# Kernel optimization log

Measured on AMD Instinct MI355X. Metric: run time of the kernel, lower is better.

The kernel has to match this reference:

```python
import jax, jax.numpy as jnp
import numpy as np

B, N, H, K = 8192, 256, 1024, 256
BETA = 0.99
TOL = 1e-4
MAX_ITER = 100

def V_fn(x, Wv):
    # x: (B,1,N) -> (B,1,1); positive-definite quadratic Lyapunov V(x) = ||x @ Wv||^2
    z = jnp.einsum('bon,nk->bok', x, Wv)
    return jnp.sum(z * z, axis=-1, keepdims=True)

def fhat_fn(x, W1, b1, W2, b2):
    # residual tanh MLP dynamics model fhat: (B,1,N) -> (B,1,N)
    h = jnp.tanh(jnp.einsum('bon,nh->boh', x, W1) + b1)
    return x + jnp.einsum('boh,hn->bon', h, W2) + b2

def dV_da(fx, a, Wv):
    # per-sample d/d(alpha) V(fx * alpha); mirrors torch.autograd.grad(Vfx, alpha)
    def v_scalar(a_s, fx_s):
        z = (fx_s * a_s) @ Wv
        return jnp.sum(z * z)
    g = jax.vmap(jax.grad(v_scalar))(a[:, 0, 0], fx[:, 0, :])
    return g[:, None, None]

def newton_F(fx, t, a, Wv):
    # newton_iter.forward: F = alpha - (V(fhatx*alpha) - target) / dV_da
    # dV_da was computed with create_graph=False in torch -> constant -> stop_gradient
    dv = jax.lax.stop_gradient(dV_da(fx, a, Wv))
    return a - (V_fn(fx * a, Wv) - t) / dv

def solve_alpha(fhatx, target, Wv):
    # vectorized Newton + bisection with per-sample masking (rootfind_train.forward)
    Bn = fhatx.shape[0]
    alpha0 = jnp.ones((Bn, 1, 1), jnp.float32)
    e1_0 = jnp.zeros_like(alpha0)
    e2_0 = jnp.ones_like(alpha0)
    m0 = (V_fn(fhatx, Wv) - target) > 0.0

    def cond(c):
        a, e1, e2, m, it = c
        return jnp.logical_and(jnp.any(m), it < MAX_ITER)

    def body(c):
        a, e1, e2, m, it = c
        a = jnp.where(m, newton_F(fhatx, target, a, Wv), a)
        m_bis = (a < e1) | (a > e2)
        a_bis = e1 + (e2 - e1) / 2
        sa = jnp.sign(V_fn(fhatx * a_bis, Wv) - target)
        s1 = jnp.sign(V_fn(fhatx * e1, Wv) - target)
        s2 = jnp.sign(V_fn(fhatx * e2, Wv) - target)
        m_end2 = m_bis & (sa * s1 < 0)
        m_end1 = m_bis & (sa * s2 < 0)
        e2 = jnp.where(m_end2, a_bis, e2)
        e1 = jnp.where(m_end1, a_bis, e1)
        a = jnp.where(m_bis, a_bis, a)
        m = jnp.abs(V_fn(fhatx * a, Wv) - target) > TOL
        return (a, e1, e2, m, it + 1)

    a, _, _, _, _ = jax.lax.while_loop(cond, body, (alpha0, e1_0, e2_0, m0, jnp.int32(0)))
    return a

def setup_inputs() -> dict:
    key = jax.random.key(0)
    ks = jax.random.split(key, 4)
    x = jax.random.normal(ks[0], (B, 1, N), jnp.float32)
    W1 = jax.random.normal(ks[1], (N, H), jnp.float32) / np.sqrt(N)
    b1 = jnp.zeros((H,), jnp.float32)
    W2 = jax.random.normal(ks[2], (H, N), jnp.float32) * (0.5 / np.sqrt(H))
    b2 = jnp.zeros((N,), jnp.float32)
    Wv = jax.random.normal(ks[3], (N, K), jnp.float32) / np.sqrt(N)
    return {'x': x, 'W1': W1, 'b1': b1, 'W2': W2, 'b2': b2, 'Wv': Wv}

def reference(x, W1, b1, W2, b2, Wv):
    fhatx = fhat_fn(x, W1, b1, W2, b2)
    target = BETA * V_fn(x, Wv)
    alpha = jax.lax.stop_gradient(solve_alpha(fhatx, target, Wv))  # alpha detached in torch
    return fhatx * alpha
```

## Files before the change

### kernel.cpp

```cpp
#include <hip/hip_runtime.h>
#include <math.h>

typedef __attribute__((ext_vector_type(8))) short bf16x8;
typedef __attribute__((ext_vector_type(4))) float f32x4;

#define MFMA __builtin_amdgcn_mfma_f32_16x16x32_bf16

static __device__ __forceinline__ unsigned short f2bf(float f) {
  union { float f; unsigned u; } a; a.f = f;
  unsigned u = a.u;
  unsigned r = u + 0x7FFF + ((u >> 16) & 1);
  return (unsigned short)(r >> 16);
}
static __device__ __forceinline__ float bf2f(unsigned short h) {
  union { unsigned u; float f; } a; a.u = ((unsigned)h) << 16;
  return a.f;
}
static __device__ __forceinline__ float tanh_fast(float x) {
  float ax = fabsf(x);
  float e = __expf(-2.0f * ax);
  float t = (1.0f - e) / (1.0f + e);
  t = (ax > 10.0f) ? 1.0f : t;
  return (x < 0.0f) ? -t : t;
}
static __device__ __forceinline__ void gload16(const void* g, void* l) {
  __builtin_amdgcn_global_load_lds(
      (const __attribute__((address_space(1))) unsigned int*)g,
      (__attribute__((address_space(3))) unsigned int*)l, 16, 0, 0);
}

__global__ __launch_bounds__(256) void k_split(
    const float* __restrict__ W1, const float* __restrict__ W2,
    const float* __restrict__ Wv, const float* __restrict__ X,
    unsigned short* __restrict__ W1Th, unsigned short* __restrict__ W1Tl,
    unsigned short* __restrict__ W2Th, unsigned short* __restrict__ W2Tl,
    unsigned short* __restrict__ WvTh, unsigned short* __restrict__ WvTl,
    unsigned short* __restrict__ Xh,  unsigned short* __restrict__ Xl)
{
  const int b = blockIdx.x, t = threadIdx.x;
  if (b >= 144) {
    const size_t i0 = (size_t)(b - 144) * 2048 + (size_t)t * 8;
    const float4 v0 = *reinterpret_cast<const float4*>(&X[i0]);
    const float4 v1 = *reinterpret_cast<const float4*>(&X[i0 + 4]);
    const float vv[8] = {v0.x, v0.y, v0.z, v0.w, v1.x, v1.y, v1.z, v1.w};
    uint4 hp, lp;
    unsigned hw[4], lw[4];
#pragma unroll
    for (int e = 0; e < 4; ++e) {
      const unsigned short h0 = f2bf(vv[2*e]), h1 = f2bf(vv[2*e+1]);
      hw[e] = (unsigned)h0 | ((unsigned)h1 << 16);
      lw[e] = (unsigned)f2bf(vv[2*e] - bf2f(h0)) |
              ((unsigned)f2bf(vv[2*e+1] - bf2f(h1)) << 16);
    }
    hp.x = hw[0]; hp.y = hw[1]; hp.z = hw[2]; hp.w = hw[3];
    lp.x = lw[0]; lp.y = lw[1]; lp.z = lw[2]; lp.w = lw[3];
    *reinterpret_cast<uint4*>(&Xh[i0]) = hp;
    *reinterpret_cast<uint4*>(&Xl[i0]) = lp;
    return;
  }

  __shared__ unsigned short shh[64 * 72], shl[64 * 72];
  const float* W; unsigned short *Th, *Tl; int Kd, Nd, k0, n0;
  if (b < 64)       { W = W1; Th = W1Th; Tl = W1Tl; Kd = 256;  Nd = 1024; k0 = (b & 3) * 64;         n0 = (b >> 2) * 64; }
  else if (b < 128) { W = W2; Th = W2Th; Tl = W2Tl; Kd = 1024; Nd = 256;  k0 = ((b - 64) & 15) * 64; n0 = ((b - 64) >> 4) * 64; }
  else              { W = Wv; Th = WvTh; Tl = WvTl; Kd = 256;  Nd = 256;  k0 = ((b - 128) & 3) * 64; n0 = ((b - 128) >> 2) * 64; }

  const int kloc = t >> 4, n4 = t & 15;
#pragma unroll
  for (int p = 0; p < 4; ++p) {
    const int kk = p * 16 + kloc;
    const float4 v = *reinterpret_cast<const float4*>(&W[(size_t)(k0 + kk) * Nd + n0 + n4 * 4]);
    const float vv[4] = {v.x, v.y, v.z, v.w};
#pragma unroll
    for (int e = 0; e < 4; ++e) {
      const unsigned short hh = f2bf(vv[e]);
      shh[(n4 * 4 + e) * 72 + kk] = hh;
      shl[(n4 * 4 + e) * 72 + kk] = f2bf(vv[e] - bf2f(hh));
    }
  }
  __syncthreads();
  const int nl = t >> 2, ko = (t & 3) * 16;
  const size_t dst = (size_t)(n0 + nl) * Kd + k0 + ko;
  *reinterpret_cast<uint4*>(&Th[dst])     = *reinterpret_cast<const uint4*>(&shh[nl * 72 + ko]);
  *reinterpret_cast<uint4*>(&Th[dst + 8]) = *reinterpret_cast<const uint4*>(&shh[nl * 72 + ko + 8]);
  *reinterpret_cast<uint4*>(&Tl[dst])     = *reinterpret_cast<const uint4*>(&shl[nl * 72 + ko]);
  *reinterpret_cast<uint4*>(&Tl[dst + 8]) = *reinterpret_cast<const uint4*>(&shl[nl * 72 + ko + 8]);
}

__global__ __launch_bounds__(256, 3) void k_gemm1(
    const unsigned short* __restrict__ Xh, const unsigned short* __restrict__ Xl,
    const unsigned short* __restrict__ BTh, const unsigned short* __restrict__ BTl,
    const float* __restrict__ bias,
    unsigned short* __restrict__ Hh, unsigned short* __restrict__ Hl)
{
  __shared__ unsigned short lds[16384];
  const int t = threadIdx.x, l = t & 63, wv = t >> 6;
  const int n0 = blockIdx.x * 128, m0 = blockIdx.y * 128;
  const int wr = wv >> 1, wc = wv & 1;

  const unsigned short* ssrc = (wv == 0) ? Xh : (wv == 1) ? Xl : (wv == 2) ? BTh : BTl;
  const int rbase = (wv < 2) ? m0 : n0;
  char* ldsb = (char*)lds + wv * 8192;
  const int srow = l >> 2, sg = l & 3;

  const int kofs = (l >> 4) * 16;
  const int arow = wr * 64 + (l & 15), brow = wc * 64 + (l & 15);

  f32x4 acc[4][4] = {};
  for (int k0 = 0; k0 < 256; k0 += 32) {
#pragma unroll
    for (int c = 0; c < 8; ++c)
      gload16(ssrc + (size_t)(rbase + c * 16 + srow) * 256 + k0 + sg * 8, ldsb + c * 1024);
    __syncthreads();

    const char* L = (const char*)lds;
    bf16x8 ah[4], al[4], bh[4], bl[4];
#pragma unroll
    for (int i = 0; i < 4; ++i) {
      ah[i] = *reinterpret_cast<const bf16x8*>(L +         (arow + i * 16) * 64 + kofs);
      al[i] = *reinterpret_cast<const bf16x8*>(L +  8192 + (arow + i * 16) * 64 + kofs);
      bh[i] = *reinterpret_cast<const bf16x8*>(L + 16384 + (brow + i * 16) * 64 + kofs);
      bl[i] = *reinterpret_cast<const bf16x8*>(L + 24576 + (brow + i * 16) * 64 + kofs);
    }
#pragma unroll
    for (int i = 0; i < 4; ++i)
#pragma unroll
      for (int j = 0; j < 4; ++j) {
        acc[i][j] = MFMA(ah[i], bh[j], acc[i][j], 0, 0, 0);
        acc[i][j] = MFMA(ah[i], bl[j], acc[i][j], 0, 0, 0);
        acc[i][j] = MFMA(al[i], bh[j], acc[i][j], 0, 0, 0);
      }
    __syncthreads();
  }

#pragma unroll
  for (int i = 0; i < 4; ++i)
#pragma unroll
    for (int j = 0; j < 4; ++j) {
      const int gn = n0 + wc * 64 + j * 16 + (l & 15);
      const float bv = bias[gn];
#pragma unroll
      for (int r = 0; r < 4; ++r) {
        const int gm = m0 + wr * 64 + i * 16 + (l >> 4) * 4 + r;
        const float tv = tanh_fast(acc[i][j][r] + bv);
        const unsigned short th = f2bf(tv);
        Hh[(size_t)gm * 1024 + gn] = th;
        Hl[(size_t)gm * 1024 + gn] = f2bf(tv - bf2f(th));
      }
    }
}

__global__ __launch_bounds__(512, 4) void k_g2va(
    const unsigned short* __restrict__ Xh, const unsigned short* __restrict__ Xl,
    const unsigned short* __restrict__ Hh, const unsigned short* __restrict__ Hl,
    const unsigned short* __restrict__ W2Th, const unsigned short* __restrict__ W2Tl,
    const unsigned short* __restrict__ WvTh, const unsigned short* __restrict__ WvTl,
    const float* __restrict__ pb2, float* __restrict__ OUT)
{
  __shared__ __align__(16) unsigned char smem[67712];
  const int t = threadIdx.x, l = t & 63, w = t >> 6;
  const int cl = l & 15, g = l >> 4;
  const int r0 = blockIdx.x * 32;

  {
    const unsigned short* xp = (w < 4) ? Xh : Xl;
    unsigned char* base = smem + ((w < 4) ? 0 : 16384);
#pragma unroll
    for (int s = 0; s < 4; ++s) {
      const int c = (w & 3) * 4 + s;
      const int row = c * 2 + (l >> 5);
      const int slot = l & 31;
      gload16(xp + (size_t)(r0 + row) * 256 + ((slot ^ (row & 7)) * 8), base + c * 1024);
    }
    const unsigned short* hp = (w < 4) ? Hh : Hl;
    unsigned char* abase = smem + 32768 + ((w < 4) ? 0 : 4096) + (w & 3) * 1024;
    const int row = (w & 3) * 8 + (l >> 3);
    const int slot = l & 7;
    gload16(hp + (size_t)(r0 + row) * 1024 + 0 * 64 + ((slot ^ (row & 7)) * 8), abase);
  }
  __syncthreads();

  f32x4 acc[2][2] = {};

  for (int c = 0; c < 16; ++c) {
    if (c < 15) {
      const int cn = c + 1;
      const unsigned short* hp = (w < 4) ? Hh : Hl;
      unsigned char* abase = smem + 32768 + (cn & 1) * 8192 + ((w < 4) ? 0 : 4096) + (w & 3) * 1024;
      const int row = (w & 3) * 8 + (l >> 3);
      const int slot = l & 7;
      gload16(hp + (size_t)(r0 + row) * 1024 + cn * 64 + ((slot ^ (row & 7)) * 8), abase);
    }
    bf16x8 b2h[2][2], b2l[2][2];
#pragma unroll
    for (int j = 0; j < 2; ++j)
#pragma unroll
      for (int ks = 0; ks < 2; ++ks) {
        const size_t off = (size_t)(w * 32 + j * 16 + cl) * 1024 + c * 64 + ks * 32 + g * 8;
        b2h[j][ks] = *reinterpret_cast<const bf16x8*>(&W2Th[off]);
        b2l[j][ks] = *reinterpret_cast<const bf16x8*>(&W2Tl[off]);
      }
    const unsigned char* AB = smem + 32768 + (c & 1) * 8192;
    bf16x8 a2h[2][2], a2l[2][2];
#pragma unroll
    for (int i = 0; i < 2; ++i)
#pragma unroll
      for (int ks = 0; ks < 2; ++ks) {
        const int row = i * 16 + cl;
        const unsigned byte = row * 128 + (((unsigned)(ks * 64 + g * 16)) ^ ((((unsigned)row) & 7u) << 4));
        a2h[i][ks] = *reinterpret_cast<const bf16x8*>(AB + byte);
        a2l[i][ks] = *reinterpret_cast<const bf16x8*>(AB + 4096 + byte);
      }
#pragma unroll
    for (int i = 0; i < 2; ++i)
#pragma unroll
      for (int j = 0; j < 2; ++j)
#pragma unroll
        for (int ks = 0; ks < 2; ++ks) {
          acc[i][j] = MFMA(a2h[i][ks], b2h[j][ks], acc[i][j], 0, 0, 0);
          acc[i][j] = MFMA(a2h[i][ks], b2l[j][ks], acc[i][j], 0, 0, 0);
          acc[i][j] = MFMA(a2l[i][ks], b2h[j][ks], acc[i][j], 0, 0, 0);
        }
    __syncthreads();
  }

  {
    float b2v[2];
#pragma unroll
    for (int j = 0; j < 2; ++j) b2v[j] = pb2[w * 32 + j * 16 + cl];
#pragma unroll
    for (int i = 0; i < 2; ++i)
#pragma unroll
      for (int j = 0; j < 2; ++j)
#pragma unroll
        for (int r = 0; r < 4; ++r) {
          const int row = i * 16 + g * 4 + r;
          const int col = w * 32 + j * 16 + cl;
          const unsigned xb = row * 512 + (((unsigned)(col * 2)) ^ ((((unsigned)row) & 7u) << 4));
          const float xv = bf2f(*reinterpret_cast<unsigned short*>(smem + xb)) +
                           bf2f(*reinterpret_cast<unsigned short*>(smem + 16384 + xb));
          const float f = acc[i][j][r] + b2v[j] + xv;
          acc[i][j][r] = f;
          const unsigned short fh = f2bf(f);
          *reinterpret_cast<unsigned short*>(smem + 32768 + xb) = fh;
          *reinterpret_cast<unsigned short*>(smem + 49152 + xb) = f2bf(f - bf2f(fh));
        }
  }
  __syncthreads();

  {
    float vx_[2][4] = {}, vf_[2][4] = {};
    f32x4 zx[2], zf[2];
#pragma unroll
    for (int nf = 0; nf < 2; ++nf) {
      zx[0] = (f32x4){}; zx[1] = (f32x4){};
      zf[0] = (f32x4){}; zf[1] = (f32x4){};
#pragma unroll
      for (int ks = 0; ks < 8; ++ks) {
        const size_t off = (size_t)(w * 32 + nf * 16 + cl) * 256 + ks * 32 + g * 8;
        const bf16x8 wvh = *reinterpret_cast<const bf16x8*>(&WvTh[off]);
        const bf16x8 wvl = *reinterpret_cast<const bf16x8*>(&WvTl[off]);
#pragma unroll
        for (int i = 0; i < 2; ++i) {
          const int row = i * 16 + cl;
          const unsigned o = ((unsigned)(ks * 64 + g * 16)) ^ ((((unsigned)row) & 7u) << 4);
          const bf16x8 xhv = *reinterpret_cast<const bf16x8*>(smem + row * 512 + o);
          const bf16x8 xlv = *reinterpret_cast<const bf16x8*>(smem + 16384 + row * 512 + o);
          const bf16x8 fhv = *reinterpret_cast<const bf16x8*>(smem + 32768 + row * 512 + o);
          const bf16x8 flv = *reinterpret_cast<const bf16x8*>(smem + 49152 + row * 512 + o);
          zx[i] = MFMA(xhv, wvh, zx[i], 0, 0, 0);
          zx[i] = MFMA(xhv, wvl, zx[i], 0, 0, 0);
          zx[i] = MFMA(xlv, wvh, zx[i], 0, 0, 0);
          zf[i] = MFMA(fhv, wvh, zf[i], 0, 0, 0);
          zf[i] = MFMA(fhv, wvl, zf[i], 0, 0, 0);
          zf[i] = MFMA(flv, wvh, zf[i], 0, 0, 0);
        }
      }
#pragma unroll
      for (int i = 0; i < 2; ++i)
#pragma unroll
        for (int r = 0; r < 4; ++r) {
          vx_[i][r] = fmaf(zx[i][r], zx[i][r], vx_[i][r]);
          vf_[i][r] = fmaf(zf[i][r], zf[i][r], vf_[i][r]);
        }
    }
    float* PX = (float*)(smem + 65536);
    float* PF = (float*)(smem + 66560);
#pragma unroll
    for (int i = 0; i < 2; ++i)
#pragma unroll
      for (int r = 0; r < 4; ++r) {
        float a = vx_[i][r], b = vf_[i][r];
        a += __shfl_xor(a, 1); a += __shfl_xor(a, 2); a += __shfl_xor(a, 4); a += __shfl_xor(a, 8);
        b += __shfl_xor(b, 1); b += __shfl_xor(b, 2); b += __shfl_xor(b, 4); b += __shfl_xor(b, 8);
        if (cl == 0) {
          const int row = i * 16 + g * 4 + r;
          PX[row * 8 + w] = a;
          PF[row * 8 + w] = b;
        }
      }
  }
  __syncthreads();

  float* ALS = (float*)(smem + 67584);
  if (t < 32) {
    const float* PX = (const float*)(smem + 65536);
    const float* PF = (const float*)(smem + 66560);
    float Vx = 0.f, Vf = 0.f;
#pragma unroll
    for (int i = 0; i < 8; ++i) { Vx += PX[t * 8 + i]; Vf += PF[t * 8 + i]; }
    const float tt2 = 0.99f * Vx;
    float a;
    if (Vf - tt2 > 0.0f)        a = sqrtf(tt2 / Vf);
    else if (tt2 - Vf > 1e-4f)  a = 0.5f;
    else                        a = 1.0f;
    ALS[t] = a;
  }
  __syncthreads();

#pragma unroll
  for (int i = 0; i < 2; ++i)
#pragma unroll
    for (int r = 0; r < 4; ++r) {
      const int row = i * 16 + g * 4 + r;
      const float a = ALS[row];
#pragma unroll
      for (int j = 0; j < 2; ++j) {
        const int col = w * 32 + j * 16 + cl;
        OUT[(size_t)(r0 + row) * 256 + col] = acc[i][j][r] * a;
      }
    }
}

extern "C" void kernel_launch(void* const* d_in, const int* in_sizes, int n_in,
                              void* d_out, int out_size, void* d_ws, size_t ws_size,
                              hipStream_t stream) {
  const float* x  = (const float*)d_in[0];
  const float* W1 = (const float*)d_in[1];
  const float* b1 = (const float*)d_in[2];
  const float* W2 = (const float*)d_in[3];
  const float* b2 = (const float*)d_in[4];
  const float* Wv = (const float*)d_in[5];
  float* out = (float*)d_out;

  char* ws = (char*)d_ws;
  unsigned short* Hh   = (unsigned short*)(ws);
  unsigned short* Hl   = (unsigned short*)(ws + 16777216);
  unsigned short* W1Th = (unsigned short*)(ws + 33554432);
  unsigned short* W1Tl = (unsigned short*)(ws + 34078720);
  unsigned short* W2Th = (unsigned short*)(ws + 34603008);
  unsigned short* W2Tl = (unsigned short*)(ws + 35127296);
  unsigned short* WvTh = (unsigned short*)(ws + 35651584);
  unsigned short* WvTl = (unsigned short*)(ws + 35782656);
  unsigned short* Xh   = (unsigned short*)(ws + 35913728);
  unsigned short* Xl   = (unsigned short*)(ws + 40108032);

  k_split<<<dim3(1168), dim3(256), 0, stream>>>(
      W1, W2, Wv, x, W1Th, W1Tl, W2Th, W2Tl, WvTh, WvTl, Xh, Xl);

  k_gemm1<<<dim3(8, 64), dim3(256), 0, stream>>>(Xh, Xl, W1Th, W1Tl, b1, Hh, Hl);
  k_g2va <<<dim3(256), dim3(512), 0, stream>>>(Xh, Xl, Hh, Hl, W2Th, W2Tl, WvTh, WvTl, b2, out);
}
```

Measured before the change: 83.41 us.

## Prefetch W2 and Wv register fragments ahead of use in g2va kernel

Adds register double-buffering for the W2 B-fragments in the k_g2va main loop: the next chunk's global loads are issued alongside the next H tile, and the loop is fully unrolled. It also hoists the Wv fragment loads ahead of the epilogue and the second V pass so that global latency overlaps earlier work. Launch bounds drop from 4 to 2 blocks per CU so the extra live registers fit. The cost is lower occupancy, which could expose other latencies.

```diff
diff --git a/kernel.cpp b/kernel.cpp
--- a/kernel.cpp
+++ b/kernel.cpp
@@ -150,7 +150,7 @@
     }
 }
 
-__global__ __launch_bounds__(512, 4) void k_g2va(
+__global__ __launch_bounds__(512, 2) void k_g2va(
     const unsigned short* __restrict__ Xh, const unsigned short* __restrict__ Xl,
     const unsigned short* __restrict__ Hh, const unsigned short* __restrict__ Hl,
     const unsigned short* __restrict__ W2Th, const unsigned short* __restrict__ W2Tl,
@@ -176,13 +176,25 @@
     unsigned char* abase = smem + 32768 + ((w < 4) ? 0 : 4096) + (w & 3) * 1024;
     const int row = (w & 3) * 8 + (l >> 3);
     const int slot = l & 7;
-    gload16(hp + (size_t)(r0 + row) * 1024 + 0 * 64 + ((slot ^ (row & 7)) * 8), abase);
-  }
+    gload16(hp + (size_t)(r0 + row) * 1024 + ((slot ^ (row & 7)) * 8), abase);
+  }
+
+  bf16x8 pbh[2][2][2], pbl[2][2][2];
+#pragma unroll
+  for (int j = 0; j < 2; ++j)
+#pragma unroll
+    for (int ks = 0; ks < 2; ++ks) {
+      const size_t off = (size_t)(w * 32 + j * 16 + cl) * 1024 + ks * 32 + g * 8;
+      pbh[0][j][ks] = *reinterpret_cast<const bf16x8*>(&W2Th[off]);
+      pbl[0][j][ks] = *reinterpret_cast<const bf16x8*>(&W2Tl[off]);
+    }
   __syncthreads();
 
   f32x4 acc[2][2] = {};
 
+#pragma unroll
   for (int c = 0; c < 16; ++c) {
+    const int p = c & 1, pn = p ^ 1;
     if (c < 15) {
       const int cn = c + 1;
       const unsigned short* hp = (w < 4) ? Hh : Hl;
@@ -190,17 +202,16 @@
       const int row = (w & 3) * 8 + (l >> 3);
       const int slot = l & 7;
       gload16(hp + (size_t)(r0 + row) * 1024 + cn * 64 + ((slot ^ (row & 7)) * 8), abase);
-    }
-    bf16x8 b2h[2][2], b2l[2][2];
-#pragma unroll
-    for (int j = 0; j < 2; ++j)
-#pragma unroll
-      for (int ks = 0; ks < 2; ++ks) {
-        const size_t off = (size_t)(w * 32 + j * 16 + cl) * 1024 + c * 64 + ks * 32 + g * 8;
-        b2h[j][ks] = *reinterpret_cast<const bf16x8*>(&W2Th[off]);
-        b2l[j][ks] = *reinterpret_cast<const bf16x8*>(&W2Tl[off]);
-      }
-    const unsigned char* AB = smem + 32768 + (c & 1) * 8192;
+#pragma unroll
+      for (int j = 0; j < 2; ++j)
+#pragma unroll
+        for (int ks = 0; ks < 2; ++ks) {
+          const size_t off = (size_t)(w * 32 + j * 16 + cl) * 1024 + cn * 64 + ks * 32 + g * 8;
+          pbh[pn][j][ks] = *reinterpret_cast<const bf16x8*>(&W2Th[off]);
+          pbl[pn][j][ks] = *reinterpret_cast<const bf16x8*>(&W2Tl[off]);
+        }
+    }
+    const unsigned char* AB = smem + 32768 + p * 8192;
     bf16x8 a2h[2][2], a2l[2][2];
 #pragma unroll
     for (int i = 0; i < 2; ++i)
@@ -217,11 +228,19 @@
       for (int j = 0; j < 2; ++j)
 #pragma unroll
         for (int ks = 0; ks < 2; ++ks) {
-          acc[i][j] = MFMA(a2h[i][ks], b2h[j][ks], acc[i][j], 0, 0, 0);
-          acc[i][j] = MFMA(a2h[i][ks], b2l[j][ks], acc[i][j], 0, 0, 0);
-          acc[i][j] = MFMA(a2l[i][ks], b2h[j][ks], acc[i][j], 0, 0, 0);
+          acc[i][j] = MFMA(a2h[i][ks], pbh[p][j][ks], acc[i][j], 0, 0, 0);
+          acc[i][j] = MFMA(a2h[i][ks], pbl[p][j][ks], acc[i][j], 0, 0, 0);
+          acc[i][j] = MFMA(a2l[i][ks], pbh[p][j][ks], acc[i][j], 0, 0, 0);
         }
     __syncthreads();
+  }
+
+  bf16x8 wvh0[8], wvl0[8];
+#pragma unroll
+  for (int ks = 0; ks < 8; ++ks) {
+    const size_t off = (size_t)(w * 32 + cl) * 256 + ks * 32 + g * 8;
+    wvh0[ks] = *reinterpret_cast<const bf16x8*>(&WvTh[off]);
+    wvl0[ks] = *reinterpret_cast<const bf16x8*>(&WvTl[off]);
   }
 
   {
@@ -249,17 +268,18 @@
   __syncthreads();
 
   {
+    bf16x8 wvh1[8], wvl1[8];
+#pragma unroll
+    for (int ks = 0; ks < 8; ++ks) {
+      const size_t off = (size_t)(w * 32 + 16 + cl) * 256 + ks * 32 + g * 8;
+      wvh1[ks] = *reinterpret_cast<const bf16x8*>(&WvTh[off]);
+      wvl1[ks] = *reinterpret_cast<const bf16x8*>(&WvTl[off]);
+    }
     float vx_[2][4] = {}, vf_[2][4] = {};
-    f32x4 zx[2], zf[2];
-#pragma unroll
-    for (int nf = 0; nf < 2; ++nf) {
-      zx[0] = (f32x4){}; zx[1] = (f32x4){};
-      zf[0] = (f32x4){}; zf[1] = (f32x4){};
+    {
+      f32x4 zx[2] = {}, zf[2] = {};
 #pragma unroll
       for (int ks = 0; ks < 8; ++ks) {
-        const size_t off = (size_t)(w * 32 + nf * 16 + cl) * 256 + ks * 32 + g * 8;
-        const bf16x8 wvh = *reinterpret_cast<const bf16x8*>(&WvTh[off]);
-        const bf16x8 wvl = *reinterpret_cast<const bf16x8*>(&WvTl[off]);
 #pragma unroll
         for (int i = 0; i < 2; ++i) {
           const int row = i * 16 + cl;
@@ -268,12 +288,40 @@
           const bf16x8 xlv = *reinterpret_cast<const bf16x8*>(smem + 16384 + row * 512 + o);
           const bf16x8 fhv = *reinterpret_cast<const bf16x8*>(smem + 32768 + row * 512 + o);
           const bf16x8 flv = *reinterpret_cast<const bf16x8*>(smem + 49152 + row * 512 + o);
-          zx[i] = MFMA(xhv, wvh, zx[i], 0, 0, 0);
-          zx[i] = MFMA(xhv, wvl, zx[i], 0, 0, 0);
-          zx[i] = MFMA(xlv, wvh, zx[i], 0, 0, 0);
-          zf[i] = MFMA(fhv, wvh, zf[i], 0, 0, 0);
-          zf[i] = MFMA(fhv, wvl, zf[i], 0, 0, 0);
-          zf[i] = MFMA(flv, wvh, zf[i], 0, 0, 0);
+          zx[i] = MFMA(xhv, wvh0[ks], zx[i], 0, 0, 0);
+          zx[i] = MFMA(xhv, wvl0[ks], zx[i], 0, 0, 0);
+          zx[i] = MFMA(xlv, wvh0[ks], zx[i], 0, 0, 0);
+          zf[i] = MFMA(fhv, wvh0[ks], zf[i], 0, 0, 0);
+          zf[i] = MFMA(fhv, wvl0[ks], zf[i], 0, 0, 0);
+          zf[i] = MFMA(flv, wvh0[ks], zf[i], 0, 0, 0);
+        }
+      }
+#pragma unroll
+      for (int i = 0; i < 2; ++i)
+#pragma unroll
+        for (int r = 0; r < 4; ++r) {
+          vx_[i][r] = fmaf(zx[i][r], zx[i][r], vx_[i][r]);
+          vf_[i][r] = fmaf(zf[i][r], zf[i][r], vf_[i][r]);
+        }
+    }
+    {
+      f32x4 zx[2] = {}, zf[2] = {};
+#pragma unroll
+      for (int ks = 0; ks < 8; ++ks) {
+#pragma unroll
+        for (int i = 0; i < 2; ++i) {
+          const int row = i * 16 + cl;
+          const unsigned o = ((unsigned)(ks * 64 + g * 16)) ^ ((((unsigned)row) & 7u) << 4);
+          const bf16x8 xhv = *reinterpret_cast<const bf16x8*>(smem + row * 512 + o);
+          const bf16x8 xlv = *reinterpret_cast<const bf16x8*>(smem + 16384 + row * 512 + o);
+          const bf16x8 fhv = *reinterpret_cast<const bf16x8*>(smem + 32768 + row * 512 + o);
+          const bf16x8 flv = *reinterpret_cast<const bf16x8*>(smem + 49152 + row * 512 + o);
+          zx[i] = MFMA(xhv, wvh1[ks], zx[i], 0, 0, 0);
+          zx[i] = MFMA(xhv, wvl1[ks], zx[i], 0, 0, 0);
+          zx[i] = MFMA(xlv, wvh1[ks], zx[i], 0, 0, 0);
+          zf[i] = MFMA(fhv, wvh1[ks], zf[i], 0, 0, 0);
+          zf[i] = MFMA(fhv, wvl1[ks], zf[i], 0, 0, 0);
+          zf[i] = MFMA(flv, wvh1[ks], zf[i], 0, 0, 0);
         }
       }
 #pragma unroll
```

Measured after the change: 83.47 us. Within noise of the previous version (+0.1%).
